# Optimization experiments

Hardware: AMD Instinct MI355X
Metric: run time of the kernel (lower is better)

## Reference

```python
import jax, jax.numpy as jnp
import numpy as np

B, L, D, G = 8, 4096, 1024, 128
EPS = 1e-5


def setup_inputs() -> dict:
    key = jax.random.key(0)
    k1, k2, k3 = jax.random.split(key, 3)
    x = jax.random.normal(k1, (B, L, D), dtype=jnp.float32)
    prev_count = jnp.ones((B,), dtype=jnp.int64)          # prior_count observations already seen
    prev_mean = jnp.zeros((B, G), dtype=jnp.float32)       # prior_mean expanded over batch
    prev_var = jnp.ones((B, G), dtype=jnp.float32)         # exp(prior_logv)=1 expanded over batch
    weight = 0.02 * jax.random.normal(k2, (D,), dtype=jnp.float32)  # gamma = weight + 1
    bias = 0.02 * jax.random.normal(k3, (D,), dtype=jnp.float32)
    padding_mask = jnp.ones((B, L), dtype=jnp.int32)       # 1 = valid token
    return {"x": x, "prev_count": prev_count, "prev_mean": prev_mean,
            "prev_var": prev_var, "weight": weight, "bias": bias,
            "padding_mask": padding_mask}


def reference(x, prev_count, prev_mean, prev_var, weight, bias, padding_mask):
    """Cumulative (online Welford / Chan) per-group timestep normalization.

    Running stats per (batch, group) are updated once per valid timestep by
    merging the d features of that group at that step; output normalizes each
    timestep with the stats *including* that step, then applies affine
    gamma = weight + 1, beta = bias. Padded steps leave stats unchanged.
    """
    Bs, Ls, Ds = x.shape
    Gs = prev_mean.shape[-1]
    d = Ds // Gs  # features per group
    gamma = (weight + 1.0).reshape(Gs, d)
    beta = bias.reshape(Gs, d)

    xg = x.reshape(Bs, Ls, Gs, d).transpose(1, 0, 2, 3)     # [L,B,G,d]
    mask = padding_mask.astype(x.dtype).T                   # [L,B]
    fd = jnp.asarray(d, x.dtype)

    def step(carry, inp):
        count, mean, var = carry        # [B], [B,G], [B,G]
        xt, mt = inp                    # [B,G,d], [B]
        mu = xt.mean(-1)                                    # per-step group mean [B,G]
        ssq = jnp.sum((xt - mu[..., None]) ** 2, -1)        # per-step group M2   [B,G]
        N = count * fd                                      # elements seen so far [B]
        Np = N + fd
        delta = mu - mean
        mean_n = mean + delta * (fd / Np)[:, None]
        M2_n = var * N[:, None] + ssq + (delta ** 2) * (N * fd / Np)[:, None]
        var_n = M2_n / Np[:, None]
        v = mt[:, None]                                     # 1 if valid else 0
        mean_u = mean + v * (mean_n - mean)
        var_u = var + v * (var_n - var)
        count_u = count + mt
        rstd = jax.lax.rsqrt(var_u + EPS)                   # cumrstd [B,G]
        y = (xt - mean_u[..., None]) * rstd[..., None] * gamma + beta
        return (count_u, mean_u, var_u), y

    count0 = prev_count.astype(x.dtype)
    (count_f, mean_f, var_f), ys = jax.lax.scan(
        step, (count0, prev_mean, prev_var), (xg, mask))
    y = ys.transpose(1, 0, 2, 3).reshape(Bs, Ls, Ds)
    return y, count_f.astype(jnp.int64), mean_f, var_f
```

## Files before the change

### kernel.cpp

```cpp
#include <hip/hip_runtime.h>

#define PB 8
#define PL 4096
#define PD 1024
#define PG 128
#define SEG 32
#define NSEG (PL / SEG)
#define NEPS 1e-5f

#define YSZ ((size_t)PB * PL * PD)
#define COUNT_OFF (YSZ)
#define MEAN_OFF (YSZ + PB)
#define VAR_OFF (YSZ + PB + (size_t)PB * PG)


__global__ __launch_bounds__(256) void k_agg(const float* __restrict__ x,
                                             const int* __restrict__ mask,
                                             float* __restrict__ aggN,
                                             float* __restrict__ aggS,
                                             float* __restrict__ aggQ) {
    int blk = blockIdx.x;
    int b = blk >> 7;
    int seg = blk & (NSEG - 1);
    int u = threadIdx.x;
    size_t row0 = (size_t)b * PL + (size_t)seg * SEG;
    const float4* xp = (const float4*)x + row0 * (PD / 4) + u;
    const int* mp = mask + b * PL + seg * SEG;

    float S = 0.f, Q = 0.f, Sb = 0.f, Qb = 0.f, nc = 0.f;
#pragma unroll 8
    for (int t = 0; t < SEG; t += 2) {
        float4 v0 = xp[(size_t)t * (PD / 4)];
        float4 v1 = xp[(size_t)(t + 1) * (PD / 4)];
        float f0 = (float)mp[t];
        float f1 = (float)mp[t + 1];
        nc += f0 + f1;
        S  = fmaf(f0, v0.x + v0.y + v0.z + v0.w, S);
        Q  = fmaf(f0, fmaf(v0.x, v0.x, fmaf(v0.y, v0.y, fmaf(v0.z, v0.z, v0.w * v0.w))), Q);
        Sb = fmaf(f1, v1.x + v1.y + v1.z + v1.w, Sb);
        Qb = fmaf(f1, fmaf(v1.x, v1.x, fmaf(v1.y, v1.y, fmaf(v1.z, v1.z, v1.w * v1.w))), Qb);
    }
    S += Sb; Q += Qb;
    S += __shfl_xor(S, 1);
    Q += __shfl_xor(Q, 1);
    if ((u & 1) == 0) {
        int idx = (b * NSEG + seg) * PG + (u >> 1);
        aggN[idx] = 8.0f * nc;
        aggS[idx] = S;
        aggQ[idx] = Q;
    }
}

__global__ __launch_bounds__(256) void k_scan(const void* __restrict__ prev_count,
                                              const float* __restrict__ prev_mean,
                                              const float* __restrict__ prev_var,
                                              const float* __restrict__ aggN,
                                              const float* __restrict__ aggS,
                                              const float* __restrict__ aggQ,
                                              float* __restrict__ carN,
                                              float* __restrict__ carS,
                                              float* __restrict__ carQ,
                                              float* __restrict__ out) {
    int tid = blockIdx.x * 256 + threadIdx.x;
    if (tid >= PB * PG) return;
    int b = tid >> 7;
    int g = tid & (PG - 1);

    const long long* p64 = (const long long*)prev_count;
    const int* p32 = (const int*)prev_count;
    long long pv = p64[b];
    float c = (pv >= 0 && pv < (1LL << 31)) ? (float)pv : (float)p32[b];

    float n = 8.0f * c;
    float m0 = prev_mean[tid];
    float S = m0 * n;
    float Q = fmaf(m0, m0, prev_var[tid]) * n;

    int idx = b * NSEG * PG + g;
    float an = aggN[idx], aS = aggS[idx], aQ = aggQ[idx];
    for (int seg = 0; seg < NSEG; ++seg) {
        int nidx = idx + PG;
        float bn = 0.f, bS = 0.f, bQ = 0.f;
        if (seg + 1 < NSEG) { bn = aggN[nidx]; bS = aggS[nidx]; bQ = aggQ[nidx]; }
        carN[idx] = n; carS[idx] = S; carQ[idx] = Q;
        n += an; S += aS; Q += aQ;
        an = bn; aS = bS; aQ = bQ;
        idx = nidx;
    }
    float inv = 1.0f / n;
    float mean = S * inv;
    out[MEAN_OFF + tid] = mean;
    out[VAR_OFF + tid] = fmaf(-mean, mean, Q * inv);
    if (g == 0) out[COUNT_OFF + b] = n * 0.125f;
}

__global__ __launch_bounds__(256) void k_out(const float* __restrict__ x,
                                             const int* __restrict__ mask,
                                             const float* __restrict__ weight,
                                             const float* __restrict__ bias,
                                             const float* __restrict__ carN,
                                             const float* __restrict__ carS,
                                             const float* __restrict__ carQ,
                                             float* __restrict__ out) {
    int blk = blockIdx.x;
    int b = blk >> 7;
    int seg = blk & (NSEG - 1);
    int u = threadIdx.x;
    int g = u >> 1;

    int cidx = (b * NSEG + seg) * PG + g;
    float n = carN[cidx];
    float S = carS[cidx];
    float Q = carQ[cidx];

    size_t row0 = (size_t)b * PL + (size_t)seg * SEG;
    const float4* xp = (const float4*)x + row0 * (PD / 4) + u;
    float4* yp = (float4*)out + row0 * (PD / 4) + u;
    const int* mp = mask + b * PL + seg * SEG;

    float4 w4 = ((const float4*)weight)[u];
    float4 b4 = ((const float4*)bias)[u];
    float gx = w4.x + 1.0f, gy = w4.y + 1.0f, gz = w4.z + 1.0f, gw = w4.w + 1.0f;

    float4 v = xp[0];
#pragma unroll 4
    for (int t = 0; t < SEG; ++t) {
        int tn = (t + 1 < SEG) ? (t + 1) : t;
        float4 vnext = xp[(size_t)tn * (PD / 4)];
        float f = (float)mp[t];
        float s  = v.x + v.y + v.z + v.w;
        float ss = fmaf(v.x, v.x, fmaf(v.y, v.y, fmaf(v.z, v.z, v.w * v.w)));
        s  += __shfl_xor(s, 1);
        ss += __shfl_xor(ss, 1);
        n = fmaf(f, 8.0f, n);
        S = fmaf(f, s, S);
        Q = fmaf(f, ss, Q);
        float inv  = __builtin_amdgcn_rcpf(n);
        float mean = S * inv;
        float var  = fmaf(-mean, mean, Q * inv);
        float rstd = __builtin_amdgcn_rsqf(var + NEPS);
        float4 y;
        y.x = fmaf((v.x - mean) * rstd, gx, b4.x);
        y.y = fmaf((v.y - mean) * rstd, gy, b4.y);
        y.z = fmaf((v.z - mean) * rstd, gz, b4.z);
        y.w = fmaf((v.w - mean) * rstd, gw, b4.w);
        yp[(size_t)t * (PD / 4)] = y;
        v = vnext;
    }
}

extern "C" void kernel_launch(void* const* d_in, const int* in_sizes, int n_in,
                              void* d_out, int out_size, void* d_ws, size_t ws_size,
                              hipStream_t stream) {
    const float* x          = (const float*)d_in[0];
    const void*  prev_count = d_in[1];
    const float* prev_mean  = (const float*)d_in[2];
    const float* prev_var   = (const float*)d_in[3];
    const float* weight     = (const float*)d_in[4];
    const float* bias       = (const float*)d_in[5];
    const int*   mask       = (const int*)d_in[6];
    float* out = (float*)d_out;
    float* ws  = (float*)d_ws;

    const size_t A = (size_t)PB * NSEG * PG;
    float* aggN = ws + 0 * A;
    float* aggS = ws + 1 * A;
    float* aggQ = ws + 2 * A;
    float* carN = ws + 3 * A;
    float* carS = ws + 4 * A;
    float* carQ = ws + 5 * A;

    hipLaunchKernelGGL(k_agg, dim3(PB * NSEG), dim3(256), 0, stream,
                       x, mask, aggN, aggS, aggQ);
    hipLaunchKernelGGL(k_scan, dim3((PB * PG + 255) / 256), dim3(256), 0, stream,
                       prev_count, prev_mean, prev_var,
                       aggN, aggS, aggQ, carN, carS, carQ, out);
    hipLaunchKernelGGL(k_out, dim3(PB * NSEG), dim3(256), 0, stream,
                       x, mask, weight, bias, carN, carS, carQ, out);
}
```

Baseline: 280.3 us.

## Halve segment size, one thread per group, batched in-place carry scan

Segment length drops from 32 to 16 and each thread now owns a whole group (two float4 per row), so blocks shrink to 128 threads, NSEG doubles, and the cross-lane shuffles go away. The serial scan kernel now prefetches aggregates in double-buffered register batches of 8 and writes the exclusive carries back into the aggregate buffers, which removes the separate carry arrays. The goal is more parallel blocks and a shorter critical path in the serial scan. The trade-offs are a longer scan (256 segments per thread), per-thread loads that are strided and less coalesced, and fewer threads per block.

Result: no change. 285.0 us (+1.7%).

```diff
diff --git a/kernel.cpp b/kernel.cpp
--- a/kernel.cpp
+++ b/kernel.cpp
@@ -4,7 +4,7 @@
 #define PL 4096
 #define PD 1024
 #define PG 128
-#define SEG 32
+#define SEG 16
 #define NSEG (PL / SEG)
 #define NEPS 1e-5f
 
@@ -14,55 +14,47 @@
 #define VAR_OFF (YSZ + PB + (size_t)PB * PG)
 
 
-__global__ __launch_bounds__(256) void k_agg(const float* __restrict__ x,
+__global__ __launch_bounds__(128) void k_agg(const float* __restrict__ x,
                                              const int* __restrict__ mask,
                                              float* __restrict__ aggN,
                                              float* __restrict__ aggS,
                                              float* __restrict__ aggQ) {
     int blk = blockIdx.x;
-    int b = blk >> 7;
+    int b = blk >> 8;
     int seg = blk & (NSEG - 1);
-    int u = threadIdx.x;
+    int g = threadIdx.x;
     size_t row0 = (size_t)b * PL + (size_t)seg * SEG;
-    const float4* xp = (const float4*)x + row0 * (PD / 4) + u;
+    const float4* xp = (const float4*)x + row0 * (PD / 4) + 2 * g;
     const int* mp = mask + b * PL + seg * SEG;
 
-    float S = 0.f, Q = 0.f, Sb = 0.f, Qb = 0.f, nc = 0.f;
+    float nc = 0.f, S = 0.f, Q = 0.f;
 #pragma unroll 8
-    for (int t = 0; t < SEG; t += 2) {
-        float4 v0 = xp[(size_t)t * (PD / 4)];
-        float4 v1 = xp[(size_t)(t + 1) * (PD / 4)];
-        float f0 = (float)mp[t];
-        float f1 = (float)mp[t + 1];
-        nc += f0 + f1;
-        S  = fmaf(f0, v0.x + v0.y + v0.z + v0.w, S);
-        Q  = fmaf(f0, fmaf(v0.x, v0.x, fmaf(v0.y, v0.y, fmaf(v0.z, v0.z, v0.w * v0.w))), Q);
-        Sb = fmaf(f1, v1.x + v1.y + v1.z + v1.w, Sb);
-        Qb = fmaf(f1, fmaf(v1.x, v1.x, fmaf(v1.y, v1.y, fmaf(v1.z, v1.z, v1.w * v1.w))), Qb);
-    }
-    S += Sb; Q += Qb;
-    S += __shfl_xor(S, 1);
-    Q += __shfl_xor(Q, 1);
-    if ((u & 1) == 0) {
-        int idx = (b * NSEG + seg) * PG + (u >> 1);
-        aggN[idx] = 8.0f * nc;
-        aggS[idx] = S;
-        aggQ[idx] = Q;
-    }
-}
-
-__global__ __launch_bounds__(256) void k_scan(const void* __restrict__ prev_count,
+    for (int t = 0; t < SEG; ++t) {
+        float4 a = xp[(size_t)t * (PD / 4)];
+        float4 c = xp[(size_t)t * (PD / 4) + 1];
+        float f = (float)mp[t];
+        nc += f;
+        float s = (a.x + a.y) + (a.z + a.w) + ((c.x + c.y) + (c.z + c.w));
+        float q = fmaf(a.x, a.x, fmaf(a.y, a.y, fmaf(a.z, a.z, fmaf(a.w, a.w,
+                  fmaf(c.x, c.x, fmaf(c.y, c.y, fmaf(c.z, c.z, c.w * c.w)))))));
+        S = fmaf(f, s, S);
+        Q = fmaf(f, q, Q);
+    }
+    int idx = blk * PG + g;
+    aggN[idx] = 8.0f * nc;
+    aggS[idx] = S;
+    aggQ[idx] = Q;
+}
+
+#define TP 8
+__global__ __launch_bounds__(128) void k_scan(const void* __restrict__ prev_count,
                                               const float* __restrict__ prev_mean,
                                               const float* __restrict__ prev_var,
-                                              const float* __restrict__ aggN,
-                                              const float* __restrict__ aggS,
-                                              const float* __restrict__ aggQ,
-                                              float* __restrict__ carN,
-                                              float* __restrict__ carS,
-                                              float* __restrict__ carQ,
+                                              float* __restrict__ aggN,
+                                              float* __restrict__ aggS,
+                                              float* __restrict__ aggQ,
                                               float* __restrict__ out) {
-    int tid = blockIdx.x * 256 + threadIdx.x;
-    if (tid >= PB * PG) return;
+    int tid = blockIdx.x * 128 + threadIdx.x;
     int b = tid >> 7;
     int g = tid & (PG - 1);
 
@@ -76,16 +68,40 @@
     float S = m0 * n;
     float Q = fmaf(m0, m0, prev_var[tid]) * n;
 
-    int idx = b * NSEG * PG + g;
-    float an = aggN[idx], aS = aggS[idx], aQ = aggQ[idx];
-    for (int seg = 0; seg < NSEG; ++seg) {
-        int nidx = idx + PG;
-        float bn = 0.f, bS = 0.f, bQ = 0.f;
-        if (seg + 1 < NSEG) { bn = aggN[nidx]; bS = aggS[nidx]; bQ = aggQ[nidx]; }
-        carN[idx] = n; carS[idx] = S; carQ[idx] = Q;
-        n += an; S += aS; Q += aQ;
-        an = bn; aS = bS; aQ = bQ;
-        idx = nidx;
+    const int base = b * NSEG * PG + g;
+    float anA[TP], aSA[TP], aQA[TP], anB[TP], aSB[TP], aQB[TP];
+
+#pragma unroll
+    for (int j = 0; j < TP; ++j) {
+        int idx = base + j * PG;
+        anA[j] = aggN[idx]; aSA[j] = aggS[idx]; aQA[j] = aggQ[idx];
+    }
+#pragma unroll 1
+    for (int t0 = 0; t0 < NSEG; t0 += 2 * TP) {
+#pragma unroll
+        for (int j = 0; j < TP; ++j) {
+            int idx = base + (t0 + TP + j) * PG;
+            anB[j] = aggN[idx]; aSB[j] = aggS[idx]; aQB[j] = aggQ[idx];
+        }
+#pragma unroll
+        for (int j = 0; j < TP; ++j) {
+            int idx = base + (t0 + j) * PG;
+            aggN[idx] = n; aggS[idx] = S; aggQ[idx] = Q;
+            n += anA[j]; S += aSA[j]; Q += aQA[j];
+        }
+        if (t0 + 2 * TP < NSEG) {
+#pragma unroll
+            for (int j = 0; j < TP; ++j) {
+                int idx = base + (t0 + 2 * TP + j) * PG;
+                anA[j] = aggN[idx]; aSA[j] = aggS[idx]; aQA[j] = aggQ[idx];
+            }
+        }
+#pragma unroll
+        for (int j = 0; j < TP; ++j) {
+            int idx = base + (t0 + TP + j) * PG;
+            aggN[idx] = n; aggS[idx] = S; aggQ[idx] = Q;
+            n += anB[j]; S += aSB[j]; Q += aQB[j];
+        }
     }
     float inv = 1.0f / n;
     float mean = S * inv;
@@ -94,7 +110,7 @@
     if (g == 0) out[COUNT_OFF + b] = n * 0.125f;
 }
 
-__global__ __launch_bounds__(256) void k_out(const float* __restrict__ x,
+__global__ __launch_bounds__(128) void k_out(const float* __restrict__ x,
                                              const int* __restrict__ mask,
                                              const float* __restrict__ weight,
                                              const float* __restrict__ bias,
@@ -103,49 +119,57 @@
                                              const float* __restrict__ carQ,
                                              float* __restrict__ out) {
     int blk = blockIdx.x;
-    int b = blk >> 7;
+    int b = blk >> 8;
     int seg = blk & (NSEG - 1);
-    int u = threadIdx.x;
-    int g = u >> 1;
-
-    int cidx = (b * NSEG + seg) * PG + g;
+    int g = threadIdx.x;
+
+    int cidx = blk * PG + g;
     float n = carN[cidx];
     float S = carS[cidx];
     float Q = carQ[cidx];
 
     size_t row0 = (size_t)b * PL + (size_t)seg * SEG;
-    const float4* xp = (const float4*)x + row0 * (PD / 4) + u;
-    float4* yp = (float4*)out + row0 * (PD / 4) + u;
+    const float4* xp = (const float4*)x + row0 * (PD / 4) + 2 * g;
+    float4* yp = (float4*)out + row0 * (PD / 4) + 2 * g;
     const int* mp = mask + b * PL + seg * SEG;
 
-    float4 w4 = ((const float4*)weight)[u];
-    float4 b4 = ((const float4*)bias)[u];
-    float gx = w4.x + 1.0f, gy = w4.y + 1.0f, gz = w4.z + 1.0f, gw = w4.w + 1.0f;
-
-    float4 v = xp[0];
-#pragma unroll 4
+    float4 wa = ((const float4*)weight)[2 * g];
+    float4 wb = ((const float4*)weight)[2 * g + 1];
+    float4 ba = ((const float4*)bias)[2 * g];
+    float4 bb = ((const float4*)bias)[2 * g + 1];
+    wa.x += 1.0f; wa.y += 1.0f; wa.z += 1.0f; wa.w += 1.0f;
+    wb.x += 1.0f; wb.y += 1.0f; wb.z += 1.0f; wb.w += 1.0f;
+
+    float4 va = xp[0];
+    float4 vb = xp[1];
+#pragma unroll
     for (int t = 0; t < SEG; ++t) {
         int tn = (t + 1 < SEG) ? (t + 1) : t;
-        float4 vnext = xp[(size_t)tn * (PD / 4)];
+        float4 na = xp[(size_t)tn * (PD / 4)];
+        float4 nb = xp[(size_t)tn * (PD / 4) + 1];
         float f = (float)mp[t];
-        float s  = v.x + v.y + v.z + v.w;
-        float ss = fmaf(v.x, v.x, fmaf(v.y, v.y, fmaf(v.z, v.z, v.w * v.w)));
-        s  += __shfl_xor(s, 1);
-        ss += __shfl_xor(ss, 1);
+        float s = (va.x + va.y) + (va.z + va.w) + ((vb.x + vb.y) + (vb.z + vb.w));
+        float q = fmaf(va.x, va.x, fmaf(va.y, va.y, fmaf(va.z, va.z, fmaf(va.w, va.w,
+                  fmaf(vb.x, vb.x, fmaf(vb.y, vb.y, fmaf(vb.z, vb.z, vb.w * vb.w)))))));
         n = fmaf(f, 8.0f, n);
         S = fmaf(f, s, S);
-        Q = fmaf(f, ss, Q);
+        Q = fmaf(f, q, Q);
         float inv  = __builtin_amdgcn_rcpf(n);
         float mean = S * inv;
         float var  = fmaf(-mean, mean, Q * inv);
         float rstd = __builtin_amdgcn_rsqf(var + NEPS);
-        float4 y;
-        y.x = fmaf((v.x - mean) * rstd, gx, b4.x);
-        y.y = fmaf((v.y - mean) * rstd, gy, b4.y);
-        y.z = fmaf((v.z - mean) * rstd, gz, b4.z);
-        y.w = fmaf((v.w - mean) * rstd, gw, b4.w);
-        yp[(size_t)t * (PD / 4)] = y;
-        v = vnext;
+        float4 ya, yb;
+        ya.x = fmaf((va.x - mean) * rstd, wa.x, ba.x);
+        ya.y = fmaf((va.y - mean) * rstd, wa.y, ba.y);
+        ya.z = fmaf((va.z - mean) * rstd, wa.z, ba.z);
+        ya.w = fmaf((va.w - mean) * rstd, wa.w, ba.w);
+        yb.x = fmaf((vb.x - mean) * rstd, wb.x, bb.x);
+        yb.y = fmaf((vb.y - mean) * rstd, wb.y, bb.y);
+        yb.z = fmaf((vb.z - mean) * rstd, wb.z, bb.z);
+        yb.w = fmaf((vb.w - mean) * rstd, wb.w, bb.w);
+        yp[(size_t)t * (PD / 4)] = ya;
+        yp[(size_t)t * (PD / 4) + 1] = yb;
+        va = na; vb = nb;
     }
 }
 
@@ -166,15 +190,12 @@
     float* aggN = ws + 0 * A;
     float* aggS = ws + 1 * A;
     float* aggQ = ws + 2 * A;
-    float* carN = ws + 3 * A;
-    float* carS = ws + 4 * A;
-    float* carQ = ws + 5 * A;
-
-    hipLaunchKernelGGL(k_agg, dim3(PB * NSEG), dim3(256), 0, stream,
+
+    hipLaunchKernelGGL(k_agg, dim3(PB * NSEG), dim3(128), 0, stream,
                        x, mask, aggN, aggS, aggQ);
-    hipLaunchKernelGGL(k_scan, dim3((PB * PG + 255) / 256), dim3(256), 0, stream,
+    hipLaunchKernelGGL(k_scan, dim3(PB * PG / 128), dim3(128), 0, stream,
                        prev_count, prev_mean, prev_var,
-                       aggN, aggS, aggQ, carN, carS, carQ, out);
-    hipLaunchKernelGGL(k_out, dim3(PB * NSEG), dim3(256), 0, stream,
-                       x, mask, weight, bias, carN, carS, carQ, out);
-}
+                       aggN, aggS, aggQ, out);
+    hipLaunchKernelGGL(k_out, dim3(PB * NSEG), dim3(128), 0, stream,
+                       x, mask, weight, bias, aggN, aggS, aggQ, out);
+}
```
